# Optimization experiments

Measured on AMD Instinct MI355X. Metric: run time of the kernel, lower is better.

Reference implementation:

```python
import jax, jax.numpy as jnp
import numpy as np

HEADS = 16
D_MODEL = 1024
D_K = D_MODEL // HEADS


def setup_inputs() -> dict:
    key = jax.random.key(0)
    ks = jax.random.split(key, 12)
    B, S = 4, 2048
    scale = 1.0 / np.sqrt(D_MODEL)
    inp = {
        'q': jax.random.normal(ks[0], (B, S, D_MODEL), jnp.float32),
        'k': jax.random.normal(ks[1], (B, S, D_MODEL), jnp.float32),
        'v': jax.random.normal(ks[2], (B, S, D_MODEL), jnp.float32),
        'Wq': jax.random.normal(ks[3], (D_MODEL, D_MODEL), jnp.float32) * scale,
        'bq': jnp.zeros((D_MODEL,), jnp.float32),
        'Wk': jax.random.normal(ks[4], (D_MODEL, D_MODEL), jnp.float32) * scale,
        'bk': jnp.zeros((D_MODEL,), jnp.float32),
        'Wv': jax.random.normal(ks[5], (D_MODEL, D_MODEL), jnp.float32) * scale,
        'bv': jnp.zeros((D_MODEL,), jnp.float32),
        'Wo': jax.random.normal(ks[6], (D_MODEL, D_MODEL), jnp.float32) * scale,
        'bo': jnp.zeros((D_MODEL,), jnp.float32),
    }
    return inp


def reference(q, k, v, Wq, bq, Wk, bk, Wv, bv, Wo, bo):
    B, S, _ = q.shape
    # linear projections, split into heads: [B, H, S, Dk]
    def proj(x, W, b):
        return (x @ W.T + b).reshape(B, -1, HEADS, D_K).transpose(0, 2, 1, 3)
    qh = proj(q, Wq, bq)
    kh = proj(k, Wk, bk)
    vh = proj(v, Wv, bv)
    scores = jnp.einsum('bhsd,bhtd->bhst', qh, kh) / jnp.sqrt(jnp.float32(D_K))
    attn = jax.nn.softmax(scores, axis=-1)
    ctx = jnp.einsum('bhst,bhtd->bhsd', attn, vh)  # [B,H,S,Dk]
    concat = ctx.transpose(0, 2, 1, 3).reshape(B, S, D_MODEL)
    return concat @ Wo.T + bo
```

## Files before the change

kernel.cpp:

```cpp
#include <hip/hip_runtime.h>
#include <hip/hip_bf16.h>


typedef __attribute__((ext_vector_type(8))) short short8;
typedef __attribute__((ext_vector_type(4))) float f32x4;
typedef __attribute__((ext_vector_type(16))) float f32x16;

#define DEV __device__ __forceinline__

DEV ushort f2bf(float f) {
  union { float f; unsigned u; } v; v.f = f;
  return (ushort)((v.u + 0x7fffu + ((v.u >> 16) & 1u)) >> 16);
}

DEV void gload_lds16(const void* g, void* lds) {
  __builtin_amdgcn_global_load_lds(
      (const __attribute__((address_space(1))) void*)g,
      (__attribute__((address_space(3))) void*)lds, 16, 0, 0);
}

__global__ void cvt_kernel(const float* __restrict__ in, ushort* __restrict__ out, int n4) {
  int stride = gridDim.x * blockDim.x;
  for (int i = blockIdx.x * blockDim.x + threadIdx.x; i < n4; i += stride) {
    float4 v = ((const float4*)in)[i];
    ushort4 o;
    o.x = f2bf(v.x); o.y = f2bf(v.y); o.z = f2bf(v.z); o.w = f2bf(v.w);
    ((ushort4*)out)[i] = o;
  }
}

__global__ void cvtw_kernel(const float* __restrict__ a, const float* __restrict__ b,
                            const float* __restrict__ c, const float* __restrict__ d,
                            ushort* __restrict__ oa, ushort* __restrict__ ob,
                            ushort* __restrict__ oc, ushort* __restrict__ od, int n4) {
  const float* s[4] = {a, b, c, d};
  ushort* o[4] = {oa, ob, oc, od};
  const float* src = s[blockIdx.y];
  ushort* dst = o[blockIdx.y];
  int stride = gridDim.x * blockDim.x;
  for (int i = blockIdx.x * blockDim.x + threadIdx.x; i < n4; i += stride) {
    float4 v = ((const float4*)src)[i];
    ushort4 u;
    u.x = f2bf(v.x); u.y = f2bf(v.y); u.z = f2bf(v.z); u.w = f2bf(v.w);
    ((ushort4*)dst)[i] = u;
  }
}

template<int MODE>
__global__ __launch_bounds__(256) void gemm_bt(
    const ushort* __restrict__ X, const ushort* __restrict__ W,
    const float* __restrict__ bias, void* __restrict__ out)
{
  constexpr int K = 1024, N = 1024;
  __shared__ __align__(16) ushort As[128 * 64];
  __shared__ __align__(16) ushort Bs[128 * 64];
  const int t = threadIdx.x;
  const int w = t >> 6, l = t & 63;
  const int bid = blockIdx.x;
  const int m0 = (bid >> 3) * 128, n0 = (bid & 7) * 128;
  const int wm = (w >> 1) * 64, wn = (w & 1) * 64;

  const f32x4 zero = {0.f, 0.f, 0.f, 0.f};
  f32x4 acc[4][4];
#pragma unroll
  for (int i = 0; i < 4; i++)
#pragma unroll
    for (int j = 0; j < 4; j++) acc[i][j] = zero;

  const int srow = t >> 3;
  const int scol = ((t & 7) ^ (srow & 7)) << 4;
  const char* xg = (const char*)X + (size_t)(m0 + srow) * 2048 + scol;
  const char* wg = (const char*)W + (size_t)(n0 + srow) * 2048 + scol;
  char* asl = (char*)As + t * 16;
  char* bsl = (char*)Bs + t * 16;

  const int swf = (l & 7) << 4;

  for (int kt = 0; kt < K; kt += 64) {
    __syncthreads();
#pragma unroll
    for (int pass = 0; pass < 4; pass++) {
      gload_lds16(xg + (size_t)pass * 32 * 2048 + kt * 2, asl + pass * 4096);
      gload_lds16(wg + (size_t)pass * 32 * 2048 + kt * 2, bsl + pass * 4096);
    }
    __syncthreads();

#pragma unroll
    for (int h = 0; h < 2; h++) {
      short8 af[4], bf[4];
#pragma unroll
      for (int i = 0; i < 4; i++) {
        int ra = wm + i * 16 + (l & 15);
        int rb = wn + i * 16 + (l & 15);
        int cb = (h * 64 + (l >> 4) * 16) ^ swf;
        af[i] = *(const short8*)((const char*)As + ra * 128 + cb);
        bf[i] = *(const short8*)((const char*)Bs + rb * 128 + cb);
      }
#pragma unroll
      for (int i = 0; i < 4; i++)
#pragma unroll
        for (int j = 0; j < 4; j++)
          acc[i][j] = __builtin_amdgcn_mfma_f32_16x16x32_bf16(af[i], bf[j], acc[i][j], 0, 0, 0);
    }
  }

#pragma unroll
  for (int i = 0; i < 4; i++) {
    int mbase = m0 + wm + i * 16 + ((l >> 4) << 2);
#pragma unroll
    for (int j = 0; j < 4; j++) {
      int n = n0 + wn + j * 16 + (l & 15);
      float bv = bias[n];
#pragma unroll
      for (int r = 0; r < 4; r++) {
        int m = mbase + r;
        float v = acc[i][j][r] + bv;
        if (MODE == 2) {
          ((float*)out)[(size_t)m * N + n] = v;
        } else {
          int b = m >> 11, s = m & 2047;
          int h = n >> 6, d = n & 63;
          size_t off;
          if (MODE == 0) off = ((size_t)(b * 16 + h) * 2048 + s) * 64 + d;
          else           off = ((size_t)(b * 16 + h) * 64 + d) * 2048 + s;
          ((ushort*)out)[off] = f2bf(v);
        }
      }
    }
  }
}

__global__ __launch_bounds__(512, 4) void attn_kernel(
    const ushort* __restrict__ Qh, const ushort* __restrict__ Kh,
    const ushort* __restrict__ Vt, ushort* __restrict__ ctx)
{
  __shared__ __align__(16) ushort Ks[2 * 64 * 64];
  __shared__ __align__(16) ushort Vs[2 * 64 * 64];
  const int t = threadIdx.x, w = t >> 6, l = t & 63;
  const int hf = l >> 5, ln = l & 31;
  const int p = blockIdx.x;
  const int logical = (p & 7) * 64 + (p >> 3);
  const int bh = logical >> 3;
  const int q0 = (logical & 7) * 256 + w * 32;
  const ushort* Qb = Qh + (size_t)bh * 2048 * 64;
  const ushort* Kb = Kh + (size_t)bh * 2048 * 64;
  const ushort* Vb = Vt + (size_t)bh * 64 * 2048;

  short8 qb[4];
  {
    const ushort* qp = Qb + (size_t)(q0 + ln) * 64 + hf * 8;
    const float SC = 0.18033688f;
#pragma unroll
    for (int s = 0; s < 4; s++) {
      short8 v = *(const short8*)(qp + s * 16);
#pragma unroll
      for (int j = 0; j < 8; j++) {
        union { float f; unsigned u; } x;
        x.u = ((unsigned)(ushort)v[j]) << 16;
        x.f *= SC;
        v[j] = (short)f2bf(x.f);
      }
      qb[s] = v;
    }
  }

  short8 ones;
#pragma unroll
  for (int j = 0; j < 8; j++) ones[j] = (short)0x3F80;

  f32x16 o_acc[2], o_l;
  f32x16 z16;
#pragma unroll
  for (int r = 0; r < 16; r++) z16[r] = 0.f;
  o_acc[0] = z16; o_acc[1] = z16; o_l = z16;

  const int srow = t >> 3;
  const int ssw = (((t & 7) ^ (srow & 7)) << 4);
  const char* kg = (const char*)Kb + (size_t)srow * 128 + ssw;
  const char* vg = (const char*)Vb + (size_t)srow * 4096 + ssw;
  char* kld = (char*)Ks + (size_t)t * 16;
  char* vld = (char*)Vs + (size_t)t * 16;

#define STAGE(buf_, kv0_) do {                                   \
    gload_lds16(kg + (size_t)(kv0_) * 128, kld + (buf_) * 8192); \
    gload_lds16(vg + (size_t)(kv0_) * 2, vld + (buf_) * 8192);   \
  } while (0)

  STAGE(0, 0);
  __syncthreads();

  const int rsw = (ln & 7) << 4;

  for (int it = 0; it < 32; it++) {
    const int cur = it & 1;
    if (it < 31) STAGE(cur ^ 1, (it + 1) * 64);
    const char* KsB = (const char*)Ks + cur * 8192;
    const char* VsB = (const char*)Vs + cur * 8192;

    f32x16 sf[2];
    __builtin_amdgcn_s_setprio(1);
#pragma unroll
    for (int f = 0; f < 2; f++) {
      f32x16 s_ = z16;
#pragma unroll
      for (int s = 0; s < 4; s++) {
        short8 kf = *(const short8*)(KsB + (32 * f + ln) * 128 + ((16 * hf + 32 * s) ^ rsw));
        s_ = __builtin_amdgcn_mfma_f32_32x32x16_bf16(kf, qb[s], s_, 0, 0, 0);
      }
      sf[f] = s_;
    }
    __builtin_amdgcn_s_setprio(0);

#pragma unroll
    for (int f = 0; f < 2; f++)
#pragma unroll
      for (int r = 0; r < 16; r++) sf[f][r] = __builtin_amdgcn_exp2f(sf[f][r]);

    __builtin_amdgcn_s_setprio(1);
#pragma unroll
    for (int f = 0; f < 2; f++) {
      unsigned wd0, wd1, wd2, wd3, wd4, wd5, wd6, wd7;
      asm("v_cvt_pk_bf16_f32 %0, %1, %2" : "=v"(wd0) : "v"(sf[f][0]),  "v"(sf[f][1]));
      asm("v_cvt_pk_bf16_f32 %0, %1, %2" : "=v"(wd1) : "v"(sf[f][2]),  "v"(sf[f][3]));
      asm("v_cvt_pk_bf16_f32 %0, %1, %2" : "=v"(wd2) : "v"(sf[f][4]),  "v"(sf[f][5]));
      asm("v_cvt_pk_bf16_f32 %0, %1, %2" : "=v"(wd3) : "v"(sf[f][6]),  "v"(sf[f][7]));
      asm("v_cvt_pk_bf16_f32 %0, %1, %2" : "=v"(wd4) : "v"(sf[f][8]),  "v"(sf[f][9]));
      asm("v_cvt_pk_bf16_f32 %0, %1, %2" : "=v"(wd5) : "v"(sf[f][10]), "v"(sf[f][11]));
      asm("v_cvt_pk_bf16_f32 %0, %1, %2" : "=v"(wd6) : "v"(sf[f][12]), "v"(sf[f][13]));
      asm("v_cvt_pk_bf16_f32 %0, %1, %2" : "=v"(wd7) : "v"(sf[f][14]), "v"(sf[f][15]));
      asm("v_permlane32_swap_b32 %0, %1" : "+v"(wd0), "+v"(wd2));
      asm("v_permlane32_swap_b32 %0, %1" : "+v"(wd1), "+v"(wd3));
      asm("v_permlane32_swap_b32 %0, %1" : "+v"(wd4), "+v"(wd6));
      asm("v_permlane32_swap_b32 %0, %1" : "+v"(wd5), "+v"(wd7));
#pragma unroll
      for (int s2 = 0; s2 < 2; s2++) {
        union { unsigned u[4]; short8 s8; } pa;
        if (s2 == 0) { pa.u[0] = wd0; pa.u[1] = wd1; pa.u[2] = wd2; pa.u[3] = wd3; }
        else         { pa.u[0] = wd4; pa.u[1] = wd5; pa.u[2] = wd6; pa.u[3] = wd7; }
        const int s = 2 * f + s2;
#pragma unroll
        for (int dn = 0; dn < 2; dn++) {
          short8 vf = *(const short8*)(VsB + (32 * dn + ln) * 128 + ((16 * hf + 32 * s) ^ rsw));
          o_acc[dn] = __builtin_amdgcn_mfma_f32_32x32x16_bf16(pa.s8, vf, o_acc[dn], 0, 0, 0);
        }
        o_l = __builtin_amdgcn_mfma_f32_32x32x16_bf16(pa.s8, ones, o_l, 0, 0, 0);
      }
    }
    __builtin_amdgcn_s_setprio(0);

    __syncthreads();
  }
#undef STAGE

  const int b = bh >> 4, hd = bh & 15;
#pragma unroll
  for (int r = 0; r < 16; r++) {
    int qrow = (r & 3) + 8 * (r >> 2) + 4 * hf;
    float inv = 1.f / o_l[r];
#pragma unroll
    for (int dn = 0; dn < 2; dn++) {
      int d = dn * 32 + ln;
      size_t off = (((size_t)b * 2048 + (q0 + qrow)) * 16 + hd) * 64 + d;
      ctx[off] = f2bf(o_acc[dn][r] * inv);
    }
  }
}

extern "C" void kernel_launch(void* const* d_in, const int* in_sizes, int n_in,
                              void* d_out, int out_size, void* d_ws, size_t ws_size,
                              hipStream_t stream) {
  const float* q  = (const float*)d_in[0];
  const float* k  = (const float*)d_in[1];
  const float* v  = (const float*)d_in[2];
  const float* Wq = (const float*)d_in[3];
  const float* bq = (const float*)d_in[4];
  const float* Wk = (const float*)d_in[5];
  const float* bk = (const float*)d_in[6];
  const float* Wv = (const float*)d_in[7];
  const float* bv = (const float*)d_in[8];
  const float* Wo = (const float*)d_in[9];
  const float* bo = (const float*)d_in[10];

  const size_t MSZ = (size_t)8192 * 1024;
  const size_t WSZ = (size_t)1024 * 1024;
  char* ws = (char*)d_ws;
  ushort* Xbuf = (ushort*)ws;
  ushort* w16[4];
  w16[0] = Xbuf + MSZ;
  w16[1] = w16[0] + WSZ;
  w16[2] = w16[1] + WSZ;
  w16[3] = w16[2] + WSZ;
  ushort* Qhb = w16[3] + WSZ;
  ushort* Khb = Qhb + MSZ;
  ushort* Vtb = Khb + MSZ;
  ushort* ctx = Xbuf;

  cvtw_kernel<<<dim3(256, 4), 256, 0, stream>>>(Wq, Wk, Wv, Wo,
                                                w16[0], w16[1], w16[2], w16[3],
                                                (int)(WSZ / 4));

  cvt_kernel<<<2048, 256, 0, stream>>>(q, Xbuf, (int)(MSZ / 4));
  gemm_bt<0><<<512, 256, 0, stream>>>(Xbuf, w16[0], bq, Qhb);
  cvt_kernel<<<2048, 256, 0, stream>>>(k, Xbuf, (int)(MSZ / 4));
  gemm_bt<0><<<512, 256, 0, stream>>>(Xbuf, w16[1], bk, Khb);
  cvt_kernel<<<2048, 256, 0, stream>>>(v, Xbuf, (int)(MSZ / 4));
  gemm_bt<1><<<512, 256, 0, stream>>>(Xbuf, w16[2], bv, Vtb);

  attn_kernel<<<dim3(512), 512, 0, stream>>>(Qhb, Khb, Vtb, ctx);

  gemm_bt<2><<<512, 256, 0, stream>>>(ctx, w16[3], bo, (float*)d_out);
}
```

Before: 213.7 us.

## Double KV tile per iteration and interleave QK of second half with PV of first

Each loop iteration now stages 128 KV rows (two 64-row sub-tiles) instead of 64, halving the number of barriers and loop trips, and doubling LDS to 64 KB per block. Inside the iteration, the QK MFMAs for the second sub-tile are issued alongside the PV MFMAs of the first, so the exp/pack of one sub-tile can overlap matrix work of the other. The added LDS and register pressure (extra packed P fragments) may reduce occupancy relative to the launch bound of 4 blocks.

```diff
diff --git a/kernel.cpp b/kernel.cpp
--- a/kernel.cpp
+++ b/kernel.cpp
@@ -134,8 +134,8 @@
     const ushort* __restrict__ Qh, const ushort* __restrict__ Kh,
     const ushort* __restrict__ Vt, ushort* __restrict__ ctx)
 {
-  __shared__ __align__(16) ushort Ks[2 * 64 * 64];
-  __shared__ __align__(16) ushort Vs[2 * 64 * 64];
+  __shared__ __align__(16) ushort Ks[2 * 2 * 64 * 64];
+  __shared__ __align__(16) ushort Vs[2 * 2 * 64 * 64];
   const int t = threadIdx.x, w = t >> 6, l = t & 63;
   const int hf = l >> 5, ln = l & 31;
   const int p = blockIdx.x;
@@ -181,9 +181,11 @@
   char* kld = (char*)Ks + (size_t)t * 16;
   char* vld = (char*)Vs + (size_t)t * 16;
 
-#define STAGE(buf_, kv0_) do {                                   \
-    gload_lds16(kg + (size_t)(kv0_) * 128, kld + (buf_) * 8192); \
-    gload_lds16(vg + (size_t)(kv0_) * 2, vld + (buf_) * 8192);   \
+#define STAGE(buf_, kv0_) do {                                              \
+    gload_lds16(kg + (size_t)(kv0_) * 128, kld + (buf_) * 16384);           \
+    gload_lds16(kg + (size_t)(kv0_) * 128 + 8192, kld + (buf_) * 16384 + 8192); \
+    gload_lds16(vg + (size_t)(kv0_) * 2, vld + (buf_) * 16384);             \
+    gload_lds16(vg + (size_t)(kv0_) * 2 + 128, vld + (buf_) * 16384 + 8192);\
   } while (0)
 
   STAGE(0, 0);
@@ -191,66 +193,87 @@
 
   const int rsw = (ln & 7) << 4;
 
-  for (int it = 0; it < 32; it++) {
+#define QK(sfv, kbase_) do {                                                \
+    _Pragma("unroll")                                                       \
+    for (int f = 0; f < 2; f++) {                                           \
+      f32x16 s_ = z16;                                                      \
+      _Pragma("unroll")                                                     \
+      for (int s = 0; s < 4; s++) {                                         \
+        short8 kf = *(const short8*)((kbase_) + (32 * f + ln) * 128 +       \
+                                     ((16 * hf + 32 * s) ^ rsw));           \
+        s_ = __builtin_amdgcn_mfma_f32_32x32x16_bf16(kf, qb[s], s_, 0, 0, 0);\
+      }                                                                     \
+      sfv[f] = s_;                                                          \
+    }                                                                       \
+  } while (0)
+
+#define EXPPACK(sfv, pav) do {                                              \
+    _Pragma("unroll")                                                       \
+    for (int f = 0; f < 2; f++) {                                           \
+      _Pragma("unroll")                                                     \
+      for (int r = 0; r < 16; r++) sfv[f][r] = __builtin_amdgcn_exp2f(sfv[f][r]); \
+      unsigned wd0, wd1, wd2, wd3, wd4, wd5, wd6, wd7;                      \
+      asm("v_cvt_pk_bf16_f32 %0, %1, %2" : "=v"(wd0) : "v"(sfv[f][0]),  "v"(sfv[f][1]));  \
+      asm("v_cvt_pk_bf16_f32 %0, %1, %2" : "=v"(wd1) : "v"(sfv[f][2]),  "v"(sfv[f][3]));  \
+      asm("v_cvt_pk_bf16_f32 %0, %1, %2" : "=v"(wd2) : "v"(sfv[f][4]),  "v"(sfv[f][5]));  \
+      asm("v_cvt_pk_bf16_f32 %0, %1, %2" : "=v"(wd3) : "v"(sfv[f][6]),  "v"(sfv[f][7]));  \
+      asm("v_cvt_pk_bf16_f32 %0, %1, %2" : "=v"(wd4) : "v"(sfv[f][8]),  "v"(sfv[f][9]));  \
+      asm("v_cvt_pk_bf16_f32 %0, %1, %2" : "=v"(wd5) : "v"(sfv[f][10]), "v"(sfv[f][11])); \
+      asm("v_cvt_pk_bf16_f32 %0, %1, %2" : "=v"(wd6) : "v"(sfv[f][12]), "v"(sfv[f][13])); \
+      asm("v_cvt_pk_bf16_f32 %0, %1, %2" : "=v"(wd7) : "v"(sfv[f][14]), "v"(sfv[f][15])); \
+      asm("v_permlane32_swap_b32 %0, %1" : "+v"(wd0), "+v"(wd2));           \
+      asm("v_permlane32_swap_b32 %0, %1" : "+v"(wd1), "+v"(wd3));           \
+      asm("v_permlane32_swap_b32 %0, %1" : "+v"(wd4), "+v"(wd6));           \
+      asm("v_permlane32_swap_b32 %0, %1" : "+v"(wd5), "+v"(wd7));           \
+      union { unsigned u[4]; short8 s8; } pk0, pk1;                         \
+      pk0.u[0] = wd0; pk0.u[1] = wd1; pk0.u[2] = wd2; pk0.u[3] = wd3;       \
+      pk1.u[0] = wd4; pk1.u[1] = wd5; pk1.u[2] = wd6; pk1.u[3] = wd7;       \
+      pav[2 * f] = pk0.s8;                                                  \
+      pav[2 * f + 1] = pk1.s8;                                              \
+    }                                                                       \
+  } while (0)
+
+#define PV(pav, vbase_) do {                                                \
+    _Pragma("unroll")                                                       \
+    for (int s = 0; s < 4; s++) {                                           \
+      _Pragma("unroll")                                                     \
+      for (int dn = 0; dn < 2; dn++) {                                      \
+        short8 vf = *(const short8*)((vbase_) + (32 * dn + ln) * 128 +      \
+                                     ((16 * hf + 32 * s) ^ rsw));           \
+        o_acc[dn] = __builtin_amdgcn_mfma_f32_32x32x16_bf16(pav[s], vf, o_acc[dn], 0, 0, 0); \
+      }                                                                     \
+      o_l = __builtin_amdgcn_mfma_f32_32x32x16_bf16(pav[s], ones, o_l, 0, 0, 0); \
+    }                                                                       \
+  } while (0)
+
+  for (int it = 0; it < 16; it++) {
     const int cur = it & 1;
-    if (it < 31) STAGE(cur ^ 1, (it + 1) * 64);
-    const char* KsB = (const char*)Ks + cur * 8192;
-    const char* VsB = (const char*)Vs + cur * 8192;
+    if (it < 15) STAGE(cur ^ 1, (it + 1) * 128);
+    const char* KsB = (const char*)Ks + cur * 16384;
+    const char* VsB = (const char*)Vs + cur * 16384;
 
     f32x16 sf[2];
+    short8 pa0[4], pa1[4];
+
     __builtin_amdgcn_s_setprio(1);
-#pragma unroll
-    for (int f = 0; f < 2; f++) {
-      f32x16 s_ = z16;
-#pragma unroll
-      for (int s = 0; s < 4; s++) {
-        short8 kf = *(const short8*)(KsB + (32 * f + ln) * 128 + ((16 * hf + 32 * s) ^ rsw));
-        s_ = __builtin_amdgcn_mfma_f32_32x32x16_bf16(kf, qb[s], s_, 0, 0, 0);
-      }
-      sf[f] = s_;
-    }
+    QK(sf, KsB);
     __builtin_amdgcn_s_setprio(0);
-
-#pragma unroll
-    for (int f = 0; f < 2; f++)
-#pragma unroll
-      for (int r = 0; r < 16; r++) sf[f][r] = __builtin_amdgcn_exp2f(sf[f][r]);
-
+    EXPPACK(sf, pa0);
     __builtin_amdgcn_s_setprio(1);
-#pragma unroll
-    for (int f = 0; f < 2; f++) {
-      unsigned wd0, wd1, wd2, wd3, wd4, wd5, wd6, wd7;
-      asm("v_cvt_pk_bf16_f32 %0, %1, %2" : "=v"(wd0) : "v"(sf[f][0]),  "v"(sf[f][1]));
-      asm("v_cvt_pk_bf16_f32 %0, %1, %2" : "=v"(wd1) : "v"(sf[f][2]),  "v"(sf[f][3]));
-      asm("v_cvt_pk_bf16_f32 %0, %1, %2" : "=v"(wd2) : "v"(sf[f][4]),  "v"(sf[f][5]));
-      asm("v_cvt_pk_bf16_f32 %0, %1, %2" : "=v"(wd3) : "v"(sf[f][6]),  "v"(sf[f][7]));
-      asm("v_cvt_pk_bf16_f32 %0, %1, %2" : "=v"(wd4) : "v"(sf[f][8]),  "v"(sf[f][9]));
-      asm("v_cvt_pk_bf16_f32 %0, %1, %2" : "=v"(wd5) : "v"(sf[f][10]), "v"(sf[f][11]));
-      asm("v_cvt_pk_bf16_f32 %0, %1, %2" : "=v"(wd6) : "v"(sf[f][12]), "v"(sf[f][13]));
-      asm("v_cvt_pk_bf16_f32 %0, %1, %2" : "=v"(wd7) : "v"(sf[f][14]), "v"(sf[f][15]));
-      asm("v_permlane32_swap_b32 %0, %1" : "+v"(wd0), "+v"(wd2));
-      asm("v_permlane32_swap_b32 %0, %1" : "+v"(wd1), "+v"(wd3));
-      asm("v_permlane32_swap_b32 %0, %1" : "+v"(wd4), "+v"(wd6));
-      asm("v_permlane32_swap_b32 %0, %1" : "+v"(wd5), "+v"(wd7));
-#pragma unroll
-      for (int s2 = 0; s2 < 2; s2++) {
-        union { unsigned u[4]; short8 s8; } pa;
-        if (s2 == 0) { pa.u[0] = wd0; pa.u[1] = wd1; pa.u[2] = wd2; pa.u[3] = wd3; }
-        else         { pa.u[0] = wd4; pa.u[1] = wd5; pa.u[2] = wd6; pa.u[3] = wd7; }
-        const int s = 2 * f + s2;
-#pragma unroll
-        for (int dn = 0; dn < 2; dn++) {
-          short8 vf = *(const short8*)(VsB + (32 * dn + ln) * 128 + ((16 * hf + 32 * s) ^ rsw));
-          o_acc[dn] = __builtin_amdgcn_mfma_f32_32x32x16_bf16(pa.s8, vf, o_acc[dn], 0, 0, 0);
-        }
-        o_l = __builtin_amdgcn_mfma_f32_32x32x16_bf16(pa.s8, ones, o_l, 0, 0, 0);
-      }
-    }
+    QK(sf, KsB + 8192);
+    PV(pa0, VsB);
     __builtin_amdgcn_s_setprio(0);
+    EXPPACK(sf, pa1);
+    __builtin_amdgcn_s_setprio(1);
+    PV(pa1, VsB + 8192);
+    __builtin_amdgcn_s_setprio(0);
 
     __syncthreads();
   }
 #undef STAGE
+#undef QK
+#undef EXPPACK
+#undef PV
 
   const int b = bh >> 4, hd = bh & 15;
 #pragma unroll
```

Result: slower. 226.0 us (+5.7%).

## Batch QKV conversion and projection into single launches, widen attention KV tile

Applied to the files above, without the earlier changes.

When the workspace is large enough, q/k/v are converted to bf16 in one 3-way kernel and the three projections run as one gemm launch with a grid of 3x512. This removes four launches and the serialization between small GEMMs, and gives better occupancy across CUs. The attention kernel now stages 128 KV rows per iteration, two 64-row sub-tiles, with double-buffered LDS of twice the size, which halves barriers and loop iterations. The cost is more workspace, larger LDS per block (possibly lower occupancy), and a fallback path when the workspace is small.

```diff
diff --git a/kernel.cpp b/kernel.cpp
--- a/kernel.cpp
+++ b/kernel.cpp
@@ -26,6 +26,23 @@
     ushort4 o;
     o.x = f2bf(v.x); o.y = f2bf(v.y); o.z = f2bf(v.z); o.w = f2bf(v.w);
     ((ushort4*)out)[i] = o;
+  }
+}
+
+__global__ void cvtx_kernel(const float* __restrict__ a, const float* __restrict__ b,
+                            const float* __restrict__ c,
+                            ushort* __restrict__ oa, ushort* __restrict__ ob,
+                            ushort* __restrict__ oc, int n4) {
+  const float* s[3] = {a, b, c};
+  ushort* o[3] = {oa, ob, oc};
+  const float* src = s[blockIdx.y];
+  ushort* dst = o[blockIdx.y];
+  int stride = gridDim.x * blockDim.x;
+  for (int i = blockIdx.x * blockDim.x + threadIdx.x; i < n4; i += stride) {
+    float4 v = ((const float4*)src)[i];
+    ushort4 u;
+    u.x = f2bf(v.x); u.y = f2bf(v.y); u.z = f2bf(v.z); u.w = f2bf(v.w);
+    ((ushort4*)dst)[i] = u;
   }
 }
 
@@ -46,12 +63,55 @@
   }
 }
 
+struct GemmAcc { f32x4 a[4][4]; };
+
+DEV void gemm_core(const ushort* X, const ushort* W, int m0, int n0,
+                   ushort* As, ushort* Bs, int t, GemmAcc& acc)
+{
+  const int w = t >> 6, l = t & 63;
+  const int wm = (w >> 1) * 64, wn = (w & 1) * 64;
+  const int srow = t >> 3;
+  const int scol = ((t & 7) ^ (srow & 7)) << 4;
+  const char* xg = (const char*)X + (size_t)(m0 + srow) * 2048 + scol;
+  const char* wg = (const char*)W + (size_t)(n0 + srow) * 2048 + scol;
+  char* asl = (char*)As + t * 16;
+  char* bsl = (char*)Bs + t * 16;
+  const int swf = (l & 7) << 4;
+
+  for (int kt = 0; kt < 1024; kt += 64) {
+    __syncthreads();
+#pragma unroll
+    for (int pass = 0; pass < 4; pass++) {
+      gload_lds16(xg + (size_t)pass * 32 * 2048 + kt * 2, asl + pass * 4096);
+      gload_lds16(wg + (size_t)pass * 32 * 2048 + kt * 2, bsl + pass * 4096);
+    }
+    __syncthreads();
+
+#pragma unroll
+    for (int h = 0; h < 2; h++) {
+      short8 af[4], bf[4];
+#pragma unroll
+      for (int i = 0; i < 4; i++) {
+        int ra = wm + i * 16 + (l & 15);
+        int rb = wn + i * 16 + (l & 15);
+        int cb = (h * 64 + (l >> 4) * 16) ^ swf;
+        af[i] = *(const short8*)((const char*)As + ra * 128 + cb);
+        bf[i] = *(const short8*)((const char*)Bs + rb * 128 + cb);
+      }
+#pragma unroll
+      for (int i = 0; i < 4; i++)
+#pragma unroll
+        for (int j = 0; j < 4; j++)
+          acc.a[i][j] = __builtin_amdgcn_mfma_f32_16x16x32_bf16(af[i], bf[j], acc.a[i][j], 0, 0, 0);
+    }
+  }
+}
+
 template<int MODE>
 __global__ __launch_bounds__(256) void gemm_bt(
     const ushort* __restrict__ X, const ushort* __restrict__ W,
     const float* __restrict__ bias, void* __restrict__ out)
 {
-  constexpr int K = 1024, N = 1024;
   __shared__ __align__(16) ushort As[128 * 64];
   __shared__ __align__(16) ushort Bs[128 * 64];
   const int t = threadIdx.x;
@@ -60,49 +120,15 @@
   const int m0 = (bid >> 3) * 128, n0 = (bid & 7) * 128;
   const int wm = (w >> 1) * 64, wn = (w & 1) * 64;
 
-  const f32x4 zero = {0.f, 0.f, 0.f, 0.f};
-  f32x4 acc[4][4];
+  GemmAcc acc;
 #pragma unroll
   for (int i = 0; i < 4; i++)
 #pragma unroll
-    for (int j = 0; j < 4; j++) acc[i][j] = zero;
-
-  const int srow = t >> 3;
-  const int scol = ((t & 7) ^ (srow & 7)) << 4;
-  const char* xg = (const char*)X + (size_t)(m0 + srow) * 2048 + scol;
-  const char* wg = (const char*)W + (size_t)(n0 + srow) * 2048 + scol;
-  char* asl = (char*)As + t * 16;
-  char* bsl = (char*)Bs + t * 16;
-
-  const int swf = (l & 7) << 4;
-
-  for (int kt = 0; kt < K; kt += 64) {
-    __syncthreads();
-#pragma unroll
-    for (int pass = 0; pass < 4; pass++) {
-      gload_lds16(xg + (size_t)pass * 32 * 2048 + kt * 2, asl + pass * 4096);
-      gload_lds16(wg + (size_t)pass * 32 * 2048 + kt * 2, bsl + pass * 4096);
-    }
-    __syncthreads();
-
-#pragma unroll
-    for (int h = 0; h < 2; h++) {
-      short8 af[4], bf[4];
-#pragma unroll
-      for (int i = 0; i < 4; i++) {
-        int ra = wm + i * 16 + (l & 15);
-        int rb = wn + i * 16 + (l & 15);
-        int cb = (h * 64 + (l >> 4) * 16) ^ swf;
-        af[i] = *(const short8*)((const char*)As + ra * 128 + cb);
-        bf[i] = *(const short8*)((const char*)Bs + rb * 128 + cb);
-      }
-#pragma unroll
-      for (int i = 0; i < 4; i++)
-#pragma unroll
-        for (int j = 0; j < 4; j++)
-          acc[i][j] = __builtin_amdgcn_mfma_f32_16x16x32_bf16(af[i], bf[j], acc[i][j], 0, 0, 0);
-    }
-  }
+    for (int j = 0; j < 4; j++)
+#pragma unroll
+      for (int r = 0; r < 4; r++) acc.a[i][j][r] = 0.f;
+
+  gemm_core(X, W, m0, n0, As, Bs, t, acc);
 
 #pragma unroll
   for (int i = 0; i < 4; i++) {
@@ -114,9 +140,9 @@
 #pragma unroll
       for (int r = 0; r < 4; r++) {
         int m = mbase + r;
-        float v = acc[i][j][r] + bv;
+        float v = acc.a[i][j][r] + bv;
         if (MODE == 2) {
-          ((float*)out)[(size_t)m * N + n] = v;
+          ((float*)out)[(size_t)m * 1024 + n] = v;
         } else {
           int b = m >> 11, s = m & 2047;
           int h = n >> 6, d = n & 63;
@@ -130,12 +156,67 @@
   }
 }
 
+__global__ __launch_bounds__(256) void gemm_qkv(
+    const ushort* __restrict__ q16, const ushort* __restrict__ k16,
+    const ushort* __restrict__ v16,
+    const ushort* __restrict__ Wq, const ushort* __restrict__ Wk,
+    const ushort* __restrict__ Wv,
+    const float* __restrict__ bq, const float* __restrict__ bk,
+    const float* __restrict__ bv,
+    ushort* __restrict__ Qhb, ushort* __restrict__ Khb, ushort* __restrict__ Vtb)
+{
+  __shared__ __align__(16) ushort As[128 * 64];
+  __shared__ __align__(16) ushort Bs[128 * 64];
+  const int y = blockIdx.y;
+  const ushort* X = (y == 0) ? q16 : (y == 1) ? k16 : v16;
+  const ushort* W = (y == 0) ? Wq : (y == 1) ? Wk : Wv;
+  const float* bias = (y == 0) ? bq : (y == 1) ? bk : bv;
+  ushort* out = (y == 0) ? Qhb : (y == 1) ? Khb : Vtb;
+
+  const int t = threadIdx.x;
+  const int w = t >> 6, l = t & 63;
+  const int bid = blockIdx.x;
+  const int m0 = (bid >> 3) * 128, n0 = (bid & 7) * 128;
+  const int wm = (w >> 1) * 64, wn = (w & 1) * 64;
+
+  GemmAcc acc;
+#pragma unroll
+  for (int i = 0; i < 4; i++)
+#pragma unroll
+    for (int j = 0; j < 4; j++)
+#pragma unroll
+      for (int r = 0; r < 4; r++) acc.a[i][j][r] = 0.f;
+
+  gemm_core(X, W, m0, n0, As, Bs, t, acc);
+
+  const bool vt = (y == 2);
+#pragma unroll
+  for (int i = 0; i < 4; i++) {
+    int mbase = m0 + wm + i * 16 + ((l >> 4) << 2);
+#pragma unroll
+    for (int j = 0; j < 4; j++) {
+      int n = n0 + wn + j * 16 + (l & 15);
+      float bv = bias[n];
+#pragma unroll
+      for (int r = 0; r < 4; r++) {
+        int m = mbase + r;
+        float v = acc.a[i][j][r] + bv;
+        int b = m >> 11, s = m & 2047;
+        int h = n >> 6, d = n & 63;
+        size_t off = vt ? ((size_t)(b * 16 + h) * 64 + d) * 2048 + s
+                        : ((size_t)(b * 16 + h) * 2048 + s) * 64 + d;
+        out[off] = f2bf(v);
+      }
+    }
+  }
+}
+
 __global__ __launch_bounds__(512, 4) void attn_kernel(
     const ushort* __restrict__ Qh, const ushort* __restrict__ Kh,
     const ushort* __restrict__ Vt, ushort* __restrict__ ctx)
 {
-  __shared__ __align__(16) ushort Ks[2 * 64 * 64];
-  __shared__ __align__(16) ushort Vs[2 * 64 * 64];
+  __shared__ __align__(16) ushort Ks[2 * 2 * 64 * 64];
+  __shared__ __align__(16) ushort Vs[2 * 2 * 64 * 64];
   const int t = threadIdx.x, w = t >> 6, l = t & 63;
   const int hf = l >> 5, ln = l & 31;
   const int p = blockIdx.x;
@@ -181,9 +262,11 @@
   char* kld = (char*)Ks + (size_t)t * 16;
   char* vld = (char*)Vs + (size_t)t * 16;
 
-#define STAGE(buf_, kv0_) do {                                   \
-    gload_lds16(kg + (size_t)(kv0_) * 128, kld + (buf_) * 8192); \
-    gload_lds16(vg + (size_t)(kv0_) * 2, vld + (buf_) * 8192);   \
+#define STAGE(buf_, kv0_) do {                                              \
+    gload_lds16(kg + (size_t)(kv0_) * 128, kld + (buf_) * 16384);           \
+    gload_lds16(kg + (size_t)(kv0_) * 128 + 8192, kld + (buf_) * 16384 + 8192); \
+    gload_lds16(vg + (size_t)(kv0_) * 2, vld + (buf_) * 16384);             \
+    gload_lds16(vg + (size_t)(kv0_) * 2 + 128, vld + (buf_) * 16384 + 8192);\
   } while (0)
 
   STAGE(0, 0);
@@ -191,62 +274,66 @@
 
   const int rsw = (ln & 7) << 4;
 
-  for (int it = 0; it < 32; it++) {
+  for (int it = 0; it < 16; it++) {
     const int cur = it & 1;
-    if (it < 31) STAGE(cur ^ 1, (it + 1) * 64);
-    const char* KsB = (const char*)Ks + cur * 8192;
-    const char* VsB = (const char*)Vs + cur * 8192;
-
-    f32x16 sf[2];
-    __builtin_amdgcn_s_setprio(1);
-#pragma unroll
-    for (int f = 0; f < 2; f++) {
-      f32x16 s_ = z16;
-#pragma unroll
-      for (int s = 0; s < 4; s++) {
-        short8 kf = *(const short8*)(KsB + (32 * f + ln) * 128 + ((16 * hf + 32 * s) ^ rsw));
-        s_ = __builtin_amdgcn_mfma_f32_32x32x16_bf16(kf, qb[s], s_, 0, 0, 0);
-      }
-      sf[f] = s_;
-    }
-    __builtin_amdgcn_s_setprio(0);
-
-#pragma unroll
-    for (int f = 0; f < 2; f++)
-#pragma unroll
-      for (int r = 0; r < 16; r++) sf[f][r] = __builtin_amdgcn_exp2f(sf[f][r]);
-
-    __builtin_amdgcn_s_setprio(1);
-#pragma unroll
-    for (int f = 0; f < 2; f++) {
-      unsigned wd0, wd1, wd2, wd3, wd4, wd5, wd6, wd7;
-      asm("v_cvt_pk_bf16_f32 %0, %1, %2" : "=v"(wd0) : "v"(sf[f][0]),  "v"(sf[f][1]));
-      asm("v_cvt_pk_bf16_f32 %0, %1, %2" : "=v"(wd1) : "v"(sf[f][2]),  "v"(sf[f][3]));
-      asm("v_cvt_pk_bf16_f32 %0, %1, %2" : "=v"(wd2) : "v"(sf[f][4]),  "v"(sf[f][5]));
-      asm("v_cvt_pk_bf16_f32 %0, %1, %2" : "=v"(wd3) : "v"(sf[f][6]),  "v"(sf[f][7]));
-      asm("v_cvt_pk_bf16_f32 %0, %1, %2" : "=v"(wd4) : "v"(sf[f][8]),  "v"(sf[f][9]));
-      asm("v_cvt_pk_bf16_f32 %0, %1, %2" : "=v"(wd5) : "v"(sf[f][10]), "v"(sf[f][11]));
-      asm("v_cvt_pk_bf16_f32 %0, %1, %2" : "=v"(wd6) : "v"(sf[f][12]), "v"(sf[f][13]));
-      asm("v_cvt_pk_bf16_f32 %0, %1, %2" : "=v"(wd7) : "v"(sf[f][14]), "v"(sf[f][15]));
-      asm("v_permlane32_swap_b32 %0, %1" : "+v"(wd0), "+v"(wd2));
-      asm("v_permlane32_swap_b32 %0, %1" : "+v"(wd1), "+v"(wd3));
-      asm("v_permlane32_swap_b32 %0, %1" : "+v"(wd4), "+v"(wd6));
-      asm("v_permlane32_swap_b32 %0, %1" : "+v"(wd5), "+v"(wd7));
-#pragma unroll
-      for (int s2 = 0; s2 < 2; s2++) {
-        union { unsigned u[4]; short8 s8; } pa;
-        if (s2 == 0) { pa.u[0] = wd0; pa.u[1] = wd1; pa.u[2] = wd2; pa.u[3] = wd3; }
-        else         { pa.u[0] = wd4; pa.u[1] = wd5; pa.u[2] = wd6; pa.u[3] = wd7; }
-        const int s = 2 * f + s2;
-#pragma unroll
-        for (int dn = 0; dn < 2; dn++) {
-          short8 vf = *(const short8*)(VsB + (32 * dn + ln) * 128 + ((16 * hf + 32 * s) ^ rsw));
-          o_acc[dn] = __builtin_amdgcn_mfma_f32_32x32x16_bf16(pa.s8, vf, o_acc[dn], 0, 0, 0);
+    if (it < 15) STAGE(cur ^ 1, (it + 1) * 128);
+
+#pragma unroll
+    for (int sub = 0; sub < 2; sub++) {
+      const char* KsB = (const char*)Ks + cur * 16384 + sub * 8192;
+      const char* VsB = (const char*)Vs + cur * 16384 + sub * 8192;
+
+      f32x16 sf[2];
+      __builtin_amdgcn_s_setprio(1);
+#pragma unroll
+      for (int f = 0; f < 2; f++) {
+        f32x16 s_ = z16;
+#pragma unroll
+        for (int s = 0; s < 4; s++) {
+          short8 kf = *(const short8*)(KsB + (32 * f + ln) * 128 + ((16 * hf + 32 * s) ^ rsw));
+          s_ = __builtin_amdgcn_mfma_f32_32x32x16_bf16(kf, qb[s], s_, 0, 0, 0);
         }
-        o_l = __builtin_amdgcn_mfma_f32_32x32x16_bf16(pa.s8, ones, o_l, 0, 0, 0);
-      }
-    }
-    __builtin_amdgcn_s_setprio(0);
+        sf[f] = s_;
+      }
+      __builtin_amdgcn_s_setprio(0);
+
+#pragma unroll
+      for (int f = 0; f < 2; f++)
+#pragma unroll
+        for (int r = 0; r < 16; r++) sf[f][r] = __builtin_amdgcn_exp2f(sf[f][r]);
+
+      __builtin_amdgcn_s_setprio(1);
+#pragma unroll
+      for (int f = 0; f < 2; f++) {
+        unsigned wd0, wd1, wd2, wd3, wd4, wd5, wd6, wd7;
+        asm("v_cvt_pk_bf16_f32 %0, %1, %2" : "=v"(wd0) : "v"(sf[f][0]),  "v"(sf[f][1]));
+        asm("v_cvt_pk_bf16_f32 %0, %1, %2" : "=v"(wd1) : "v"(sf[f][2]),  "v"(sf[f][3]));
+        asm("v_cvt_pk_bf16_f32 %0, %1, %2" : "=v"(wd2) : "v"(sf[f][4]),  "v"(sf[f][5]));
+        asm("v_cvt_pk_bf16_f32 %0, %1, %2" : "=v"(wd3) : "v"(sf[f][6]),  "v"(sf[f][7]));
+        asm("v_cvt_pk_bf16_f32 %0, %1, %2" : "=v"(wd4) : "v"(sf[f][8]),  "v"(sf[f][9]));
+        asm("v_cvt_pk_bf16_f32 %0, %1, %2" : "=v"(wd5) : "v"(sf[f][10]), "v"(sf[f][11]));
+        asm("v_cvt_pk_bf16_f32 %0, %1, %2" : "=v"(wd6) : "v"(sf[f][12]), "v"(sf[f][13]));
+        asm("v_cvt_pk_bf16_f32 %0, %1, %2" : "=v"(wd7) : "v"(sf[f][14]), "v"(sf[f][15]));
+        asm("v_permlane32_swap_b32 %0, %1" : "+v"(wd0), "+v"(wd2));
+        asm("v_permlane32_swap_b32 %0, %1" : "+v"(wd1), "+v"(wd3));
+        asm("v_permlane32_swap_b32 %0, %1" : "+v"(wd4), "+v"(wd6));
+        asm("v_permlane32_swap_b32 %0, %1" : "+v"(wd5), "+v"(wd7));
+#pragma unroll
+        for (int s2 = 0; s2 < 2; s2++) {
+          union { unsigned u[4]; short8 s8; } pa;
+          if (s2 == 0) { pa.u[0] = wd0; pa.u[1] = wd1; pa.u[2] = wd2; pa.u[3] = wd3; }
+          else         { pa.u[0] = wd4; pa.u[1] = wd5; pa.u[2] = wd6; pa.u[3] = wd7; }
+          const int s = 2 * f + s2;
+#pragma unroll
+          for (int dn = 0; dn < 2; dn++) {
+            short8 vf = *(const short8*)(VsB + (32 * dn + ln) * 128 + ((16 * hf + 32 * s) ^ rsw));
+            o_acc[dn] = __builtin_amdgcn_mfma_f32_32x32x16_bf16(pa.s8, vf, o_acc[dn], 0, 0, 0);
+          }
+          o_l = __builtin_amdgcn_mfma_f32_32x32x16_bf16(pa.s8, ones, o_l, 0, 0, 0);
+        }
+      }
+      __builtin_amdgcn_s_setprio(0);
+    }
 
     __syncthreads();
   }
@@ -284,29 +371,51 @@
   const size_t MSZ = (size_t)8192 * 1024;
   const size_t WSZ = (size_t)1024 * 1024;
   char* ws = (char*)d_ws;
-  ushort* Xbuf = (ushort*)ws;
-  ushort* w16[4];
-  w16[0] = Xbuf + MSZ;
-  w16[1] = w16[0] + WSZ;
-  w16[2] = w16[1] + WSZ;
-  w16[3] = w16[2] + WSZ;
-  ushort* Qhb = w16[3] + WSZ;
-  ushort* Khb = Qhb + MSZ;
-  ushort* Vtb = Khb + MSZ;
-  ushort* ctx = Xbuf;
-
-  cvtw_kernel<<<dim3(256, 4), 256, 0, stream>>>(Wq, Wk, Wv, Wo,
-                                                w16[0], w16[1], w16[2], w16[3],
-                                                (int)(WSZ / 4));
-
-  cvt_kernel<<<2048, 256, 0, stream>>>(q, Xbuf, (int)(MSZ / 4));
-  gemm_bt<0><<<512, 256, 0, stream>>>(Xbuf, w16[0], bq, Qhb);
-  cvt_kernel<<<2048, 256, 0, stream>>>(k, Xbuf, (int)(MSZ / 4));
-  gemm_bt<0><<<512, 256, 0, stream>>>(Xbuf, w16[1], bk, Khb);
-  cvt_kernel<<<2048, 256, 0, stream>>>(v, Xbuf, (int)(MSZ / 4));
-  gemm_bt<1><<<512, 256, 0, stream>>>(Xbuf, w16[2], bv, Vtb);
-
-  attn_kernel<<<dim3(512), 512, 0, stream>>>(Qhb, Khb, Vtb, ctx);
-
-  gemm_bt<2><<<512, 256, 0, stream>>>(ctx, w16[3], bo, (float*)d_out);
-}
+
+  if (ws_size >= (size_t)(104 + 2) * 1024 * 1024) {
+    ushort* qb16 = (ushort*)ws;
+    ushort* kb16 = qb16 + MSZ;
+    ushort* vb16 = kb16 + MSZ;
+    ushort* w16_0 = vb16 + MSZ;
+    ushort* w16_1 = w16_0 + WSZ;
+    ushort* w16_2 = w16_1 + WSZ;
+    ushort* w16_3 = w16_2 + WSZ;
+    ushort* Qhb = w16_3 + WSZ;
+    ushort* Khb = Qhb + MSZ;
+    ushort* Vtb = Khb + MSZ;
+    ushort* ctx = qb16;
+
+    cvtw_kernel<<<dim3(256, 4), 256, 0, stream>>>(Wq, Wk, Wv, Wo,
+                                                  w16_0, w16_1, w16_2, w16_3,
+                                                  (int)(WSZ / 4));
+    cvtx_kernel<<<dim3(1024, 3), 256, 0, stream>>>(q, k, v, qb16, kb16, vb16,
+                                                   (int)(MSZ / 4));
+    gemm_qkv<<<dim3(512, 3), 256, 0, stream>>>(qb16, kb16, vb16,
+                                               w16_0, w16_1, w16_2,
+                                               bq, bk, bv, Qhb, Khb, Vtb);
+    attn_kernel<<<dim3(512), 512, 0, stream>>>(Qhb, Khb, Vtb, ctx);
+    gemm_bt<2><<<512, 256, 0, stream>>>(ctx, w16_3, bo, (float*)d_out);
+  } else {
+    ushort* Xbuf = (ushort*)ws;
+    ushort* w16_0 = Xbuf + MSZ;
+    ushort* w16_1 = w16_0 + WSZ;
+    ushort* w16_2 = w16_1 + WSZ;
+    ushort* w16_3 = w16_2 + WSZ;
+    ushort* Qhb = w16_3 + WSZ;
+    ushort* Khb = Qhb + MSZ;
+    ushort* Vtb = Khb + MSZ;
+    ushort* ctx = Xbuf;
+
+    cvtw_kernel<<<dim3(256, 4), 256, 0, stream>>>(Wq, Wk, Wv, Wo,
+                                                  w16_0, w16_1, w16_2, w16_3,
+                                                  (int)(WSZ / 4));
+    cvt_kernel<<<2048, 256, 0, stream>>>(q, Xbuf, (int)(MSZ / 4));
+    gemm_bt<0><<<512, 256, 0, stream>>>(Xbuf, w16_0, bq, Qhb);
+    cvt_kernel<<<2048, 256, 0, stream>>>(k, Xbuf, (int)(MSZ / 4));
+    gemm_bt<0><<<512, 256, 0, stream>>>(Xbuf, w16_1, bk, Khb);
+    cvt_kernel<<<2048, 256, 0, stream>>>(v, Xbuf, (int)(MSZ / 4));
+    gemm_bt<1><<<512, 256, 0, stream>>>(Xbuf, w16_2, bv, Vtb);
+    attn_kernel<<<dim3(512), 512, 0, stream>>>(Qhb, Khb, Vtb, ctx);
+    gemm_bt<2><<<512, 256, 0, stream>>>(ctx, w16_3, bo, (float*)d_out);
+  }
+}
```

New measurement: 213.7 us. Within noise of the previous version (+0.0%).
